# Kernel tuning notes

Measured on AMD Instinct MI355X. Metric: run time of the kernel, lower is better.

The kernel has to match this reference:

```python
import jax, jax.numpy as jnp
import numpy as np

B, N, D, H, K_OUT, NCLUST = 8, 4096, 3, 256, 1024, 63


def setup_inputs() -> dict:
    key = jax.random.key(0)
    ks = jax.random.split(key, 16)

    def lin_w(k, out_d, in_d):
        return jax.random.normal(k, (out_d, in_d), jnp.float32) / np.float32(np.sqrt(in_d))

    def lin_b(k, out_d):
        return jax.random.normal(k, (out_d,), jnp.float32) * 0.01

    x = jax.random.normal(ks[0], (B, N, D), jnp.float32)
    # DBSCAN-style labels: -1 = noise, 0..NCLUST-1 cluster ids
    labels = jax.random.randint(ks[1], (B, N), -1, NCLUST)
    return {
        "x": x,
        "labels": labels,
        "Wq": lin_w(ks[2], D, D), "bq": lin_b(ks[3], D),
        "Wk": lin_w(ks[4], D, D), "bk": lin_b(ks[5], D),
        "Wv": lin_w(ks[6], D, D), "bv": lin_b(ks[7], D),
        "Wo": lin_w(ks[8], D, D), "bo": lin_b(ks[9], D),
        "W1": lin_w(ks[10], H, D), "b1": lin_b(ks[11], H),
        "W2": lin_w(ks[12], D, H), "b2": lin_b(ks[13], D),
    }


def reference(x, labels, Wq, bq, Wk, bk, Wv, bv, Wo, bo, W1, b1, W2, b2):
    # Projections are per-point linear maps; computing them on all points is
    # identical to per-cluster gathers in the original.
    q = x @ Wq.T + bq  # [B,N,D]
    k = x @ Wk.T + bk
    v = x @ Wv.T + bv

    scale = 1.0 / np.float32(np.sqrt(x.shape[-1]))  # SDPA default 1/sqrt(E)
    scores = jnp.einsum('bnd,bmd->bnm', q, k) * scale  # [B,N,N]

    valid = labels != -1  # noise points produce zero output
    # Block-diagonal mask: attend only within the same (non-noise) cluster.
    same = (labels[:, :, None] == labels[:, None, :]) & valid[:, :, None]
    scores = jnp.where(same, scores, jnp.float32(-1e9))
    attn = jax.nn.softmax(scores, axis=-1)
    ctx = jnp.einsum('bnm,bmd->bnd', attn, v)
    ctx = jnp.where(valid[:, :, None], ctx, 0.0)  # outputs stay zero for noise

    out = ctx @ Wo.T + bo  # out_proj applied to all rows (incl. zeroed noise rows)
    h = jax.nn.relu(out @ W1.T + b1)
    y = h @ W2.T + b2  # [B,N,D]
    return y[:, :K_OUT]  # stack of transformed[:K]
```

## Files before the change

### kernel.cpp

```cpp
#include <hip/hip_runtime.h>

#define BB 8
#define NN 4096
#define HH 256
#define KOUT 1024
#define NC 64

__global__ __launch_bounds__(1024) void k_prep(
    const float* __restrict__ x, const int* __restrict__ labels,
    const float* __restrict__ Wq, const float* __restrict__ bq,
    const float* __restrict__ Wk, const float* __restrict__ bk,
    const float* __restrict__ Wv, const float* __restrict__ bv,
    float4* __restrict__ k4, float4* __restrict__ v4, float4* __restrict__ q4,
    int* __restrict__ counts, int* __restrict__ offsets, int* __restrict__ members)
{
    int b = blockIdx.x;
    int tid = threadIdx.x;
    __shared__ int hist[NC], cur[NC];
    if (tid < NC) hist[tid] = 0;
    __syncthreads();

    const int* lb = labels + b * NN;
    const float* xb = x + b * NN * 3;

    #pragma unroll
    for (int kk = 0; kk < 4; kk++) {
        int i = kk * 1024 + tid;
        float x0 = xb[i * 3 + 0];
        float x1 = xb[i * 3 + 1];
        float x2 = xb[i * 3 + 2];

        float k0 = bk[0] + x0 * Wk[0] + x1 * Wk[1] + x2 * Wk[2];
        float k1 = bk[1] + x0 * Wk[3] + x1 * Wk[4] + x2 * Wk[5];
        float k2 = bk[2] + x0 * Wk[6] + x1 * Wk[7] + x2 * Wk[8];
        k4[b * NN + i] = make_float4(k0, k1, k2, 0.f);

        float v0 = bv[0] + x0 * Wv[0] + x1 * Wv[1] + x2 * Wv[2];
        float v1 = bv[1] + x0 * Wv[3] + x1 * Wv[4] + x2 * Wv[5];
        float v2 = bv[2] + x0 * Wv[6] + x1 * Wv[7] + x2 * Wv[8];
        v4[b * NN + i] = make_float4(v0, v1, v2, 0.f);

        if (i < KOUT) {
            float q0 = bq[0] + x0 * Wq[0] + x1 * Wq[1] + x2 * Wq[2];
            float q1 = bq[1] + x0 * Wq[3] + x1 * Wq[4] + x2 * Wq[5];
            float q2 = bq[2] + x0 * Wq[6] + x1 * Wq[7] + x2 * Wq[8];
            q4[b * KOUT + i] = make_float4(q0, q1, q2, 0.f);
        }

        int l = lb[i];
        if (l >= 0) atomicAdd(&hist[l], 1);
    }
    __syncthreads();

    if (tid < 64) {
        int v = hist[tid];
        int s = v;
        #pragma unroll
        for (int d = 1; d < 64; d <<= 1) {
            int o = __shfl_up(s, d, 64);
            if (tid >= d) s += o;
        }
        int e = s - v;
        cur[tid] = e;
        counts[b * NC + tid]  = v;
        offsets[b * NC + tid] = e;
    }
    __syncthreads();

    #pragma unroll
    for (int kk = 0; kk < 4; kk++) {
        int i = kk * 1024 + tid;
        int l = lb[i];
        if (l >= 0) {
            int p = atomicAdd(&cur[l], 1);
            members[b * NN + p] = i;
        }
    }
}

__global__ __launch_bounds__(256) void k_attn(
    const int* __restrict__ labels,
    const float4* __restrict__ k4, const float4* __restrict__ v4,
    const float4* __restrict__ q4,
    const int* __restrict__ counts, const int* __restrict__ offsets,
    const int* __restrict__ members,
    const float* __restrict__ Wo, const float* __restrict__ bo,
    const float* __restrict__ W1, const float* __restrict__ b1,
    const float* __restrict__ W2, const float* __restrict__ b2,
    float* __restrict__ out)
{
    int row  = (blockIdx.x * 256 + threadIdx.x) >> 6;
    int lane = threadIdx.x & 63;
    int b = row >> 10, n = row & (KOUT - 1);
    int l = labels[b * NN + n];

    float c0 = 0.f, c1 = 0.f, c2 = 0.f;
    if (l >= 0) {
        float4 q = q4[row];
        const float scale = 0.5773502691896258f;
        int base = offsets[b * NC + l];
        int cnt  = counts[b * NC + l];
        const int* mem = members + b * NN + base;
        const float4* kb = k4 + b * NN;
        const float4* vb = v4 + b * NN;

        float m = -1e30f;
        for (int i = lane; i < cnt; i += 64) {
            float4 k = kb[mem[i]];
            float s = (q.x * k.x + q.y * k.y + q.z * k.z) * scale;
            m = fmaxf(m, s);
        }
        #pragma unroll
        for (int d = 32; d > 0; d >>= 1) m = fmaxf(m, __shfl_xor(m, d, 64));

        float denom = 0.f;
        for (int i = lane; i < cnt; i += 64) {
            int idx = mem[i];
            float4 k = kb[idx];
            float s = (q.x * k.x + q.y * k.y + q.z * k.z) * scale;
            float w = __expf(s - m);
            float4 v = vb[idx];
            denom += w;
            c0 += w * v.x; c1 += w * v.y; c2 += w * v.z;
        }
        #pragma unroll
        for (int d = 32; d > 0; d >>= 1) {
            denom += __shfl_xor(denom, d, 64);
            c0    += __shfl_xor(c0, d, 64);
            c1    += __shfl_xor(c1, d, 64);
            c2    += __shfl_xor(c2, d, 64);
        }
        float inv = 1.f / denom;
        c0 *= inv; c1 *= inv; c2 *= inv;
    }

    float o0 = bo[0] + c0 * Wo[0] + c1 * Wo[1] + c2 * Wo[2];
    float o1 = bo[1] + c0 * Wo[3] + c1 * Wo[4] + c2 * Wo[5];
    float o2 = bo[2] + c0 * Wo[6] + c1 * Wo[7] + c2 * Wo[8];

    float y0 = 0.f, y1 = 0.f, y2 = 0.f;
    #pragma unroll
    for (int t = 0; t < 4; t++) {
        int j = lane + 64 * t;
        float h = fmaxf(W1[j * 3 + 0] * o0 + W1[j * 3 + 1] * o1 + W1[j * 3 + 2] * o2 + b1[j], 0.f);
        y0 += h * W2[j];
        y1 += h * W2[HH + j];
        y2 += h * W2[2 * HH + j];
    }
    #pragma unroll
    for (int d = 32; d > 0; d >>= 1) {
        y0 += __shfl_xor(y0, d, 64);
        y1 += __shfl_xor(y1, d, 64);
        y2 += __shfl_xor(y2, d, 64);
    }
    if (lane == 0) {
        out[row * 3 + 0] = y0 + b2[0];
        out[row * 3 + 1] = y1 + b2[1];
        out[row * 3 + 2] = y2 + b2[2];
    }
}

extern "C" void kernel_launch(void* const* d_in, const int* in_sizes, int n_in,
                              void* d_out, int out_size, void* d_ws, size_t ws_size,
                              hipStream_t stream) {
    const float* x      = (const float*)d_in[0];
    const int*   labels = (const int*)d_in[1];
    const float* Wq = (const float*)d_in[2];
    const float* bq = (const float*)d_in[3];
    const float* Wk = (const float*)d_in[4];
    const float* bk = (const float*)d_in[5];
    const float* Wv = (const float*)d_in[6];
    const float* bv = (const float*)d_in[7];
    const float* Wo = (const float*)d_in[8];
    const float* bo = (const float*)d_in[9];
    const float* W1 = (const float*)d_in[10];
    const float* b1 = (const float*)d_in[11];
    const float* W2 = (const float*)d_in[12];
    const float* b2 = (const float*)d_in[13];
    float* out = (float*)d_out;

    float4* k4 = (float4*)d_ws;
    float4* v4 = k4 + BB * NN;
    float4* q4 = v4 + BB * NN;
    int* counts  = (int*)(q4 + BB * KOUT);
    int* offsets = counts + BB * NC;
    int* members = offsets + BB * NC;

    k_prep<<<BB, 1024, 0, stream>>>(x, labels, Wq, bq, Wk, bk, Wv, bv,
                                    k4, v4, q4, counts, offsets, members);
    k_attn<<<(BB * KOUT * 64) / 256, 256, 0, stream>>>(labels, k4, v4, q4, counts, offsets, members,
                                                       Wo, bo, W1, b1, W2, b2, out);
}
```

Before: 98.89 us.

## Split prep kernel into many-block projection and scatter kernels with global atomics

Replaces the 8-block prep kernel with two 128-block kernels: one computes projections and per-block label histograms merged into global counts via atomics, and a second computes prefix offsets per block and scatters member indices using global atomic cursors. A memset zeroes counts and cursors first. The goal is to spread the serial-ish prep work across many CUs instead of 8. The cost is an extra launch plus a memset, and global atomic contention. Member order within a cluster becomes nondeterministic, which only affects float summation order.

```diff
diff --git a/kernel.cpp b/kernel.cpp
--- a/kernel.cpp
+++ b/kernel.cpp
@@ -6,75 +6,78 @@
 #define KOUT 1024
 #define NC 64
 
-__global__ __launch_bounds__(1024) void k_prep(
+__global__ __launch_bounds__(256) void k_proj(
     const float* __restrict__ x, const int* __restrict__ labels,
     const float* __restrict__ Wq, const float* __restrict__ bq,
     const float* __restrict__ Wk, const float* __restrict__ bk,
     const float* __restrict__ Wv, const float* __restrict__ bv,
     float4* __restrict__ k4, float4* __restrict__ v4, float4* __restrict__ q4,
-    int* __restrict__ counts, int* __restrict__ offsets, int* __restrict__ members)
+    int* __restrict__ counts)
 {
-    int b = blockIdx.x;
-    int tid = threadIdx.x;
-    __shared__ int hist[NC], cur[NC];
-    if (tid < NC) hist[tid] = 0;
+    int t = blockIdx.x * 256 + threadIdx.x;
+    int b = t >> 12, n = t & (NN - 1);
+
+    __shared__ int hist[NC];
+    if (threadIdx.x < NC) hist[threadIdx.x] = 0;
     __syncthreads();
 
-    const int* lb = labels + b * NN;
-    const float* xb = x + b * NN * 3;
+    float x0 = x[t * 3 + 0];
+    float x1 = x[t * 3 + 1];
+    float x2 = x[t * 3 + 2];
 
-    #pragma unroll
-    for (int kk = 0; kk < 4; kk++) {
-        int i = kk * 1024 + tid;
-        float x0 = xb[i * 3 + 0];
-        float x1 = xb[i * 3 + 1];
-        float x2 = xb[i * 3 + 2];
+    float k0 = bk[0] + x0 * Wk[0] + x1 * Wk[1] + x2 * Wk[2];
+    float k1 = bk[1] + x0 * Wk[3] + x1 * Wk[4] + x2 * Wk[5];
+    float k2 = bk[2] + x0 * Wk[6] + x1 * Wk[7] + x2 * Wk[8];
+    k4[t] = make_float4(k0, k1, k2, 0.f);
 
-        float k0 = bk[0] + x0 * Wk[0] + x1 * Wk[1] + x2 * Wk[2];
-        float k1 = bk[1] + x0 * Wk[3] + x1 * Wk[4] + x2 * Wk[5];
-        float k2 = bk[2] + x0 * Wk[6] + x1 * Wk[7] + x2 * Wk[8];
-        k4[b * NN + i] = make_float4(k0, k1, k2, 0.f);
+    float v0 = bv[0] + x0 * Wv[0] + x1 * Wv[1] + x2 * Wv[2];
+    float v1 = bv[1] + x0 * Wv[3] + x1 * Wv[4] + x2 * Wv[5];
+    float v2 = bv[2] + x0 * Wv[6] + x1 * Wv[7] + x2 * Wv[8];
+    v4[t] = make_float4(v0, v1, v2, 0.f);
 
-        float v0 = bv[0] + x0 * Wv[0] + x1 * Wv[1] + x2 * Wv[2];
-        float v1 = bv[1] + x0 * Wv[3] + x1 * Wv[4] + x2 * Wv[5];
-        float v2 = bv[2] + x0 * Wv[6] + x1 * Wv[7] + x2 * Wv[8];
-        v4[b * NN + i] = make_float4(v0, v1, v2, 0.f);
+    if (n < KOUT) {
+        float q0 = bq[0] + x0 * Wq[0] + x1 * Wq[1] + x2 * Wq[2];
+        float q1 = bq[1] + x0 * Wq[3] + x1 * Wq[4] + x2 * Wq[5];
+        float q2 = bq[2] + x0 * Wq[6] + x1 * Wq[7] + x2 * Wq[8];
+        q4[b * KOUT + n] = make_float4(q0, q1, q2, 0.f);
+    }
 
-        if (i < KOUT) {
-            float q0 = bq[0] + x0 * Wq[0] + x1 * Wq[1] + x2 * Wq[2];
-            float q1 = bq[1] + x0 * Wq[3] + x1 * Wq[4] + x2 * Wq[5];
-            float q2 = bq[2] + x0 * Wq[6] + x1 * Wq[7] + x2 * Wq[8];
-            q4[b * KOUT + i] = make_float4(q0, q1, q2, 0.f);
-        }
+    int l = labels[t];
+    if (l >= 0) atomicAdd(&hist[l], 1);
+    __syncthreads();
+    if (threadIdx.x < NC) {
+        int h = hist[threadIdx.x];
+        if (h > 0) atomicAdd(&counts[b * NC + threadIdx.x], h);
+    }
+}
 
-        int l = lb[i];
-        if (l >= 0) atomicAdd(&hist[l], 1);
-    }
-    __syncthreads();
+__global__ __launch_bounds__(256) void k_scat(
+    const int* __restrict__ labels, const int* __restrict__ counts,
+    int* __restrict__ offsets, int* __restrict__ cur,
+    int* __restrict__ members)
+{
+    int t = blockIdx.x * 256 + threadIdx.x;
+    int b = t >> 12, n = t & (NN - 1);
 
-    if (tid < 64) {
-        int v = hist[tid];
+    __shared__ int offs[NC];
+    if (threadIdx.x < 64) {
+        int v = counts[b * NC + threadIdx.x];
         int s = v;
         #pragma unroll
         for (int d = 1; d < 64; d <<= 1) {
             int o = __shfl_up(s, d, 64);
-            if (tid >= d) s += o;
+            if (threadIdx.x >= d) s += o;
         }
         int e = s - v;
-        cur[tid] = e;
-        counts[b * NC + tid]  = v;
-        offsets[b * NC + tid] = e;
+        offs[threadIdx.x] = e;
+        if ((blockIdx.x & 15) == 0) offsets[b * NC + threadIdx.x] = e;
     }
     __syncthreads();
 
-    #pragma unroll
-    for (int kk = 0; kk < 4; kk++) {
-        int i = kk * 1024 + tid;
-        int l = lb[i];
-        if (l >= 0) {
-            int p = atomicAdd(&cur[l], 1);
-            members[b * NN + p] = i;
-        }
+    int l = labels[t];
+    if (l >= 0) {
+        int p = offs[l] + atomicAdd(&cur[b * NC + l], 1);
+        members[b * NN + p] = n;
     }
 }
 
@@ -183,11 +186,14 @@
     float4* v4 = k4 + BB * NN;
     float4* q4 = v4 + BB * NN;
     int* counts  = (int*)(q4 + BB * KOUT);
-    int* offsets = counts + BB * NC;
+    int* cur     = counts + BB * NC;
+    int* offsets = cur + BB * NC;
     int* members = offsets + BB * NC;
 
-    k_prep<<<BB, 1024, 0, stream>>>(x, labels, Wq, bq, Wk, bk, Wv, bv,
-                                    k4, v4, q4, counts, offsets, members);
+    hipMemsetAsync(counts, 0, 2 * BB * NC * sizeof(int), stream);
+    k_proj<<<(BB * NN) / 256, 256, 0, stream>>>(x, labels, Wq, bq, Wk, bk, Wv, bv,
+                                                k4, v4, q4, counts);
+    k_scat<<<(BB * NN) / 256, 256, 0, stream>>>(labels, counts, offsets, cur, members);
     k_attn<<<(BB * KOUT * 64) / 256, 256, 0, stream>>>(labels, k4, v4, q4, counts, offsets, members,
                                                        Wo, bo, W1, b1, W2, b2, out);
 }
```

Measured after the change: 103.6 us. 4.8% more time.

## Split cluster build across 128 blocks and recompute K/V inline in attention

Applied to the files above, without the earlier changes.

The single-block-per-batch prep kernel is replaced by a 128-block build kernel that makes per-segment histograms and member lists. The attention kernel merges the 16 segment lists with a wave-level scan and binary search, and recomputes q/k/v from x on the fly instead of reading precomputed float4 buffers. The max-subtraction pass of softmax is dropped, so the scores are exponentiated directly. This removes the serial 8-block prep bottleneck and one pass over the keys, but adds per-element search shuffles, redundant projection math, and a risk of overflow if scores are large.

```diff
diff --git a/kernel.cpp b/kernel.cpp
--- a/kernel.cpp
+++ b/kernel.cpp
@@ -5,85 +5,54 @@
 #define HH 256
 #define KOUT 1024
 #define NC 64
+#define NSEG 16
+#define SEG 256
 
-__global__ __launch_bounds__(1024) void k_prep(
-    const float* __restrict__ x, const int* __restrict__ labels,
-    const float* __restrict__ Wq, const float* __restrict__ bq,
-    const float* __restrict__ Wk, const float* __restrict__ bk,
-    const float* __restrict__ Wv, const float* __restrict__ bv,
-    float4* __restrict__ k4, float4* __restrict__ v4, float4* __restrict__ q4,
-    int* __restrict__ counts, int* __restrict__ offsets, int* __restrict__ members)
+__global__ __launch_bounds__(256) void k_build(
+    const int* __restrict__ labels,
+    int* __restrict__ counts,
+    int* __restrict__ offs,
+    int* __restrict__ members)
 {
-    int b = blockIdx.x;
-    int tid = threadIdx.x;
+    int t = blockIdx.x * 256 + threadIdx.x;
+    int b  = t >> 12;
+    int sb = (t >> 8) & (NSEG - 1);
+    int n  = t & (NN - 1);
+    int l  = labels[t];
+
     __shared__ int hist[NC], cur[NC];
-    if (tid < NC) hist[tid] = 0;
+    if (threadIdx.x < NC) hist[threadIdx.x] = 0;
     __syncthreads();
-
-    const int* lb = labels + b * NN;
-    const float* xb = x + b * NN * 3;
-
-    #pragma unroll
-    for (int kk = 0; kk < 4; kk++) {
-        int i = kk * 1024 + tid;
-        float x0 = xb[i * 3 + 0];
-        float x1 = xb[i * 3 + 1];
-        float x2 = xb[i * 3 + 2];
-
-        float k0 = bk[0] + x0 * Wk[0] + x1 * Wk[1] + x2 * Wk[2];
-        float k1 = bk[1] + x0 * Wk[3] + x1 * Wk[4] + x2 * Wk[5];
-        float k2 = bk[2] + x0 * Wk[6] + x1 * Wk[7] + x2 * Wk[8];
-        k4[b * NN + i] = make_float4(k0, k1, k2, 0.f);
-
-        float v0 = bv[0] + x0 * Wv[0] + x1 * Wv[1] + x2 * Wv[2];
-        float v1 = bv[1] + x0 * Wv[3] + x1 * Wv[4] + x2 * Wv[5];
-        float v2 = bv[2] + x0 * Wv[6] + x1 * Wv[7] + x2 * Wv[8];
-        v4[b * NN + i] = make_float4(v0, v1, v2, 0.f);
-
-        if (i < KOUT) {
-            float q0 = bq[0] + x0 * Wq[0] + x1 * Wq[1] + x2 * Wq[2];
-            float q1 = bq[1] + x0 * Wq[3] + x1 * Wq[4] + x2 * Wq[5];
-            float q2 = bq[2] + x0 * Wq[6] + x1 * Wq[7] + x2 * Wq[8];
-            q4[b * KOUT + i] = make_float4(q0, q1, q2, 0.f);
-        }
-
-        int l = lb[i];
-        if (l >= 0) atomicAdd(&hist[l], 1);
-    }
+    if (l >= 0) atomicAdd(&hist[l], 1);
     __syncthreads();
-
-    if (tid < 64) {
-        int v = hist[tid];
+    if (threadIdx.x < NC) {
+        int v = hist[threadIdx.x];
         int s = v;
         #pragma unroll
         for (int d = 1; d < 64; d <<= 1) {
             int o = __shfl_up(s, d, 64);
-            if (tid >= d) s += o;
+            if (threadIdx.x >= d) s += o;
         }
         int e = s - v;
-        cur[tid] = e;
-        counts[b * NC + tid]  = v;
-        offsets[b * NC + tid] = e;
+        int gi = (b * NSEG + sb) * NC + threadIdx.x;
+        counts[gi] = v;
+        offs[gi]   = e;
+        cur[threadIdx.x] = e;
     }
     __syncthreads();
-
-    #pragma unroll
-    for (int kk = 0; kk < 4; kk++) {
-        int i = kk * 1024 + tid;
-        int l = lb[i];
-        if (l >= 0) {
-            int p = atomicAdd(&cur[l], 1);
-            members[b * NN + p] = i;
-        }
+    if (l >= 0) {
+        int p = atomicAdd(&cur[l], 1);
+        members[b * NN + sb * SEG + p] = n;
     }
 }
 
 __global__ __launch_bounds__(256) void k_attn(
-    const int* __restrict__ labels,
-    const float4* __restrict__ k4, const float4* __restrict__ v4,
-    const float4* __restrict__ q4,
-    const int* __restrict__ counts, const int* __restrict__ offsets,
+    const float* __restrict__ x, const int* __restrict__ labels,
+    const int* __restrict__ counts, const int* __restrict__ offs,
     const int* __restrict__ members,
+    const float* __restrict__ Wq, const float* __restrict__ bq,
+    const float* __restrict__ Wk, const float* __restrict__ bk,
+    const float* __restrict__ Wv, const float* __restrict__ bv,
     const float* __restrict__ Wo, const float* __restrict__ bo,
     const float* __restrict__ W1, const float* __restrict__ b1,
     const float* __restrict__ W2, const float* __restrict__ b2,
@@ -94,43 +63,64 @@
     int b = row >> 10, n = row & (KOUT - 1);
     int l = labels[b * NN + n];
 
+    const float* xr = x + (b * NN + n) * 3;
+    float x0 = xr[0], x1 = xr[1], x2 = xr[2];
+    float q0 = bq[0] + x0 * Wq[0] + x1 * Wq[1] + x2 * Wq[2];
+    float q1 = bq[1] + x0 * Wq[3] + x1 * Wq[4] + x2 * Wq[5];
+    float q2 = bq[2] + x0 * Wq[6] + x1 * Wq[7] + x2 * Wq[8];
+
     float c0 = 0.f, c1 = 0.f, c2 = 0.f;
     if (l >= 0) {
-        float4 q = q4[row];
         const float scale = 0.5773502691896258f;
-        int base = offsets[b * NC + l];
-        int cnt  = counts[b * NC + l];
-        const int* mem = members + b * NN + base;
-        const float4* kb = k4 + b * NN;
-        const float4* vb = v4 + b * NN;
+        int s16 = lane & (NSEG - 1);
+        int gi = (b * NSEG + s16) * NC + l;
+        int cs = counts[gi];
+        int start = b * NN + s16 * SEG + offs[gi];
+        int p = cs;
+        #pragma unroll
+        for (int d = 1; d < 16; d <<= 1) {
+            int o = __shfl_up(p, d, 16);
+            if (s16 >= d) p += o;
+        }
+        int e = p - cs;
+        int T = __shfl(p, 15, 64);
 
-        float m = -1e30f;
-        for (int i = lane; i < cnt; i += 64) {
-            float4 k = kb[mem[i]];
-            float s = (q.x * k.x + q.y * k.y + q.z * k.z) * scale;
-            m = fmaxf(m, s);
-        }
-        #pragma unroll
-        for (int d = 32; d > 0; d >>= 1) m = fmaxf(m, __shfl_xor(m, d, 64));
-
-        float denom = 0.f;
-        for (int i = lane; i < cnt; i += 64) {
-            int idx = mem[i];
-            float4 k = kb[idx];
-            float s = (q.x * k.x + q.y * k.y + q.z * k.z) * scale;
-            float w = __expf(s - m);
-            float4 v = vb[idx];
-            denom += w;
-            c0 += w * v.x; c1 += w * v.y; c2 += w * v.z;
+        float dsum = 0.f;
+        int iters = (T + 63) >> 6;
+        for (int it = 0; it < iters; ++it) {
+            int i = lane + (it << 6);
+            bool act = i < T;
+            int ic = act ? i : (T - 1);
+            int lo = 0;
+            #pragma unroll
+            for (int step = 8; step >= 1; step >>= 1) {
+                int cand = lo + step;
+                int ev = __shfl(e, cand, 64);
+                lo = (ev <= ic) ? cand : lo;
+            }
+            int eo  = __shfl(e, lo, 64);
+            int bse = __shfl(start, lo, 64);
+            int m = members[bse + (ic - eo)];
+            const float* xm = x + (b * NN + m) * 3;
+            float y0 = xm[0], y1 = xm[1], y2 = xm[2];
+            float k0 = bk[0] + y0 * Wk[0] + y1 * Wk[1] + y2 * Wk[2];
+            float k1 = bk[1] + y0 * Wk[3] + y1 * Wk[4] + y2 * Wk[5];
+            float k2 = bk[2] + y0 * Wk[6] + y1 * Wk[7] + y2 * Wk[8];
+            float sc = (q0 * k0 + q1 * k1 + q2 * k2) * scale;
+            float w = act ? __expf(sc) : 0.f;
+            float v0 = bv[0] + y0 * Wv[0] + y1 * Wv[1] + y2 * Wv[2];
+            float v1 = bv[1] + y0 * Wv[3] + y1 * Wv[4] + y2 * Wv[5];
+            float v2 = bv[2] + y0 * Wv[6] + y1 * Wv[7] + y2 * Wv[8];
+            dsum += w; c0 += w * v0; c1 += w * v1; c2 += w * v2;
         }
         #pragma unroll
         for (int d = 32; d > 0; d >>= 1) {
-            denom += __shfl_xor(denom, d, 64);
-            c0    += __shfl_xor(c0, d, 64);
-            c1    += __shfl_xor(c1, d, 64);
-            c2    += __shfl_xor(c2, d, 64);
+            dsum += __shfl_xor(dsum, d, 64);
+            c0   += __shfl_xor(c0, d, 64);
+            c1   += __shfl_xor(c1, d, 64);
+            c2   += __shfl_xor(c2, d, 64);
         }
-        float inv = 1.f / denom;
+        float inv = 1.f / dsum;
         c0 *= inv; c1 *= inv; c2 *= inv;
     }
 
@@ -179,15 +169,12 @@
     const float* b2 = (const float*)d_in[13];
     float* out = (float*)d_out;
 
-    float4* k4 = (float4*)d_ws;
-    float4* v4 = k4 + BB * NN;
-    float4* q4 = v4 + BB * NN;
-    int* counts  = (int*)(q4 + BB * KOUT);
-    int* offsets = counts + BB * NC;
-    int* members = offsets + BB * NC;
+    int* counts  = (int*)d_ws;
+    int* offs    = counts + BB * NSEG * NC;
+    int* members = offs + BB * NSEG * NC;
 
-    k_prep<<<BB, 1024, 0, stream>>>(x, labels, Wq, bq, Wk, bk, Wv, bv,
-                                    k4, v4, q4, counts, offsets, members);
-    k_attn<<<(BB * KOUT * 64) / 256, 256, 0, stream>>>(labels, k4, v4, q4, counts, offsets, members,
+    k_build<<<(BB * NN) / 256, 256, 0, stream>>>(labels, counts, offs, members);
+    k_attn<<<(BB * KOUT * 64) / 256, 256, 0, stream>>>(x, labels, counts, offs, members,
+                                                       Wq, bq, Wk, bk, Wv, bv,
                                                        Wo, bo, W1, b1, W2, b2, out);
 }
```

New measurement: 93.32 us. 5.6% less time.
